# Kernel optimization log

Measured on AMD Instinct MI355X. Metric: run time of the kernel, lower is better.

## Reference

```python
import jax, jax.numpy as jnp
import numpy as np

N, D, H, E = 50000, 128, 128, 800000

def _layernorm(h, g, b, eps=1e-5):
    m = jnp.mean(h, axis=-1, keepdims=True)
    v = jnp.mean((h - m) ** 2, axis=-1, keepdims=True)
    return (h - m) * jax.lax.rsqrt(v + eps) * g + b

def setup_inputs() -> dict:
    key = jax.random.key(0)
    ks = jax.random.split(key, 24)
    s = 0.02
    inp = {
        "x": jax.random.normal(ks[0], (N, D), dtype=jnp.float32),
        "edge_index": jax.random.randint(ks[1], (2, E), 0, N, dtype=jnp.int64),
        "degree": jax.random.uniform(ks[2], (N, 1), dtype=jnp.float32) * 32.0,
        "W_lin": jax.random.normal(ks[3], (D, H), jnp.float32) * s,
        "b_lin": jnp.zeros((H,), jnp.float32),
        "Wa1": jax.random.normal(ks[4], (H, H), jnp.float32) * s,
        "ba1": jnp.zeros((H,), jnp.float32),
        "Wa2": jax.random.normal(ks[5], (H, H), jnp.float32) * s,
        "ba2": jnp.zeros((H,), jnp.float32),
        "Wb1": jax.random.normal(ks[6], (H, H), jnp.float32) * s,
        "bb1": jnp.zeros((H,), jnp.float32),
        "Wb2": jax.random.normal(ks[7], (H, H), jnp.float32) * s,
        "bb2": jnp.zeros((H,), jnp.float32),
        "Wg1": jax.random.normal(ks[8], (H, H), jnp.float32) * s,
        "bg1": jnp.zeros((H,), jnp.float32),
        "Wg2": jax.random.normal(ks[9], (H, H), jnp.float32) * s,
        "bg2": jnp.zeros((H,), jnp.float32),
        "Wf1": jax.random.normal(ks[10], (H, H), jnp.float32) * s,
        "bf1": jnp.zeros((H,), jnp.float32),
        "Wf2": jax.random.normal(ks[11], (H, H), jnp.float32) * s,
        "bf2": jnp.zeros((H,), jnp.float32),
        "ln_g": jnp.ones((H,), jnp.float32),
        "ln_b": jnp.zeros((H,), jnp.float32),
    }
    return inp

def reference(x, edge_index, degree, W_lin, b_lin, Wa1, ba1, Wa2, ba2,
              Wb1, bb1, Wb2, bb2, Wg1, bg1, Wg2, bg2, Wf1, bf1, Wf2, bf2,
              ln_g, ln_b):
    # Dropout layers are identity (eval mode)
    h = x @ W_lin + b_lin                                  # [N,H]
    x_res = _layernorm(h, ln_g, ln_b)
    alpha = jax.nn.softplus(jax.nn.relu(h @ Wa1 + ba1) @ Wa2 + ba2)
    beta = jax.nn.softplus(jax.nn.relu(h @ Wb1 + bb1) @ Wb2 + bb2)
    gamma = jax.nn.gelu(h @ Wg1 + bg1, approximate=False) @ Wg2 + bg2
    src, dst = edge_index[0], edge_index[1]
    agg = jax.ops.segment_sum(h[src], dst, num_segments=h.shape[0])  # [N,H]
    y = (beta * agg + gamma) / (alpha + beta * degree)
    z = jax.nn.gelu(y @ Wf1 + bf1, approximate=False) @ Wf2 + bf2
    return z + x_res
```

## Files before the change

### kernel.cpp

```cpp
#include <hip/hip_runtime.h>
#include <hip/hip_bf16.h>
#include <math.h>

#define NODES 50000
#define NEDGE 800000
#define NBLK_SCAN ((NODES + 255) / 256)
#define NT_TILES 782
#define NR_BLK 1563

typedef __bf16 bf16_t;
typedef __bf16 bf16x8 __attribute__((ext_vector_type(8)));
typedef float floatx4 __attribute__((ext_vector_type(4)));

__device__ __forceinline__ float bfbits2f(unsigned int hi16) {
    union { unsigned int u; float f; } c; c.u = hi16; return c.f;
}
__device__ __forceinline__ unsigned short f2bfbits(float f) {
    bf16_t b = (bf16_t)f; unsigned short u;
    __builtin_memcpy(&u, &b, 2); return u;
}

__device__ __forceinline__ float act_rt(float v, int act) {
    if (act == 1) return fmaxf(v, 0.f);
    if (act == 2) {
        float w = 0.79788456f * (v + 0.044715f * v * v * v);
        float e = __expf(2.f * w);
        float th = 1.f - 2.f / (e + 1.f);
        return 0.5f * v * (1.f + th);
    }
    if (act == 3) return fmaxf(v, 0.f) + __logf(1.f + __expf(-fabsf(v)));
    return v;
}

__global__ __launch_bounds__(256) void prep_w_zero(
    const float* __restrict__ w0, const float* __restrict__ w1,
    const float* __restrict__ w2, const float* __restrict__ w3,
    const float* __restrict__ w4, const float* __restrict__ w5,
    const float* __restrict__ w6, const float* __restrict__ w7,
    const float* __restrict__ w8, bf16_t* __restrict__ wt,
    int* __restrict__ cnt)
{
    if (blockIdx.x >= 9) {
        int i = (blockIdx.x - 9) * 256 + threadIdx.x;
        if (i < NODES) cnt[i] = 0;
        return;
    }
    const float* Ws[9] = {w0, w1, w2, w3, w4, w5, w6, w7, w8};
    const float* W = Ws[blockIdx.x];
    bf16_t* o = wt + blockIdx.x * 16384;
    for (int idx = threadIdx.x; idx < 16384; idx += 256) {
        int k = idx >> 7, n = idx & 127;
        o[n * 128 + k] = (bf16_t)W[idx];
    }
}

__device__ __forceinline__ void load_w_regs(const bf16_t* __restrict__ W,
                                            uint4 (&wr)[8], int t)
{
    for (int i = 0; i < 8; ++i) {
        int c = t + i * 256;
        int row = c >> 4, g = c & 15;
        wr[i] = *(const uint4*)(W + row * 128 + g * 8);
    }
}
__device__ __forceinline__ void store_w_regs(const uint4 (&wr)[8],
                                             bf16_t* Bs, int t)
{
    for (int i = 0; i < 8; ++i) {
        int c = t + i * 256;
        int row = c >> 4, g = c & 15;
        *(uint4*)&Bs[row * 128 + ((g ^ (row & 15)) * 8)] = wr[i];
    }
}
__device__ __forceinline__ void afrag_gbf16(const bf16_t* __restrict__ A,
        bf16x8 (&af)[4], int r0, int lane, int wave, int M)
{
    int gr = r0 + wave * 16 + (lane & 15);
    gr = min(gr, M - 1);
    const bf16_t* p = A + (size_t)gr * 128 + (lane >> 4) * 8;
    for (int kc = 0; kc < 4; ++kc)
        af[kc] = *(const bf16x8*)(p + kc * 32);
}
__device__ __forceinline__ void kloop64(const bf16x8 (&af)[4], const bf16_t* Bs,
                                        floatx4 (&acc)[8], int l15, int quad)
{
    for (int ni = 0; ni < 8; ++ni)
        for (int r = 0; r < 4; ++r) acc[ni][r] = 0.f;
    for (int kc = 0; kc < 4; ++kc) {
        int kg = kc * 4 + quad;
        bf16x8 b[8];
        for (int ni = 0; ni < 8; ++ni) {
            int row = ni * 16 + l15;
            b[ni] = *(const bf16x8*)&Bs[row * 128 + ((kg ^ l15) * 8)];
        }
        for (int ni = 0; ni < 8; ++ni)
            acc[ni] = __builtin_amdgcn_mfma_f32_16x16x32_bf16(
                af[kc], b[ni], acc[ni], 0, 0, 0);
    }
}
__device__ __forceinline__ void write_Csw(bf16_t* Csw, floatx4 (&acc)[8],
        const float (&bias_r)[8], int lane, int wave, int act)
{
    const int l15 = lane & 15, quad = lane >> 4;
    for (int ni = 0; ni < 8; ++ni) {
        int col = ni * 16 + l15;
        for (int r = 0; r < 4; ++r) {
            int row = wave * 16 + quad * 4 + r;
            float v = act_rt(acc[ni][r] + bias_r[ni], act);
            Csw[row * 128 + (((col >> 3) ^ (row & 15)) << 3) + (col & 7)] = (bf16_t)v;
        }
    }
}
__device__ __forceinline__ void afrag_Csw(const bf16_t* Csw, bf16x8 (&af)[4],
                                          int lane, int wave)
{
    int l15 = lane & 15, quad = lane >> 4;
    int row = wave * 16 + l15;
    for (int kc = 0; kc < 4; ++kc) {
        int kg = kc * 4 + quad;
        af[kc] = *(const bf16x8*)&Csw[row * 128 + ((kg ^ l15) * 8)];
    }
}
__device__ __forceinline__ void copy_Csw_out(const bf16_t* Csw,
        bf16_t* __restrict__ out, int t, int r0, int M)
{
    for (int i = 0; i < 4; ++i) {
        int c = t + i * 256;
        int row = c >> 4, g = c & 15;
        int gr = r0 + row;
        if (gr < M)
            *(uint4*)(out + (size_t)gr * 128 + g * 8) =
                *(const uint4*)&Csw[row * 128 + ((g ^ (row & 15)) * 8)];
    }
}

__global__ __launch_bounds__(256, 3) void hln_hist(
    const float* __restrict__ x, const bf16_t* __restrict__ wt,
    const float* __restrict__ b_lin,
    const float* __restrict__ ln_g, const float* __restrict__ ln_b,
    bf16_t* __restrict__ h, bf16_t* __restrict__ xres,
    const int* __restrict__ ei, int* __restrict__ cnt, int M)
{
    __shared__ __align__(16) char smem[49152];
    const int t = threadIdx.x;
    const int g = blockIdx.x >> 1;

    if (blockIdx.x & 1) {
        int base = g * 1024;
        for (int i = 0; i < 4; ++i) {
            int e = base + i * 256 + t;
            if (e < NEDGE) atomicAdd(&cnt[ei[NEDGE + e]], 1);
        }
        return;
    }

    bf16_t* Bs  = (bf16_t*)smem;
    bf16_t* Csw = (bf16_t*)(smem + 32768);
    const int r0 = g * 64;
    const int lane = t & 63, wave = t >> 6, l15 = lane & 15, quad = lane >> 4;
    uint4 wr[8];
    bf16x8 af[4];
    floatx4 acc[8];
    float bias_r[8];
    for (int ni = 0; ni < 8; ++ni) bias_r[ni] = b_lin[ni * 16 + l15];

    {
        int gr = min(r0 + wave * 16 + l15, M - 1);
        const float* p = x + (size_t)gr * 128 + quad * 8;
        for (int kc = 0; kc < 4; ++kc) {
            float4 u0 = *(const float4*)(p + kc * 32);
            float4 u1 = *(const float4*)(p + kc * 32 + 4);
            bf16x8 f;
            f[0] = (bf16_t)u0.x; f[1] = (bf16_t)u0.y;
            f[2] = (bf16_t)u0.z; f[3] = (bf16_t)u0.w;
            f[4] = (bf16_t)u1.x; f[5] = (bf16_t)u1.y;
            f[6] = (bf16_t)u1.z; f[7] = (bf16_t)u1.w;
            af[kc] = f;
        }
    }
    load_w_regs(wt, wr, t);
    store_w_regs(wr, Bs, t);
    __syncthreads();
    kloop64(af, Bs, acc, l15, quad);
    write_Csw(Csw, acc, bias_r, lane, wave, 0);
    __syncthreads();

    int row = t >> 2, p4 = t & 3;
    int gr = r0 + row;
    uint4 raw[4];
    float vals[32];
    float s = 0.f, sq = 0.f;
    for (int i = 0; i < 4; ++i) {
        int lg = p4 * 4 + i;
        raw[i] = *(const uint4*)&Csw[row * 128 + ((lg ^ (row & 15)) * 8)];
        const unsigned* u = (const unsigned*)&raw[i];
        for (int k = 0; k < 4; ++k) {
            float f0 = bfbits2f(u[k] << 16);
            float f1 = bfbits2f(u[k] & 0xffff0000u);
            vals[i * 8 + k * 2] = f0; vals[i * 8 + k * 2 + 1] = f1;
            s += f0 + f1; sq += f0 * f0 + f1 * f1;
        }
    }
    s += __shfl_xor(s, 1, 64);  sq += __shfl_xor(sq, 1, 64);
    s += __shfl_xor(s, 2, 64);  sq += __shfl_xor(sq, 2, 64);
    float m   = s * (1.f / 128.f);
    float var = fmaxf(sq * (1.f / 128.f) - m * m, 0.f);
    float rs  = rsqrtf(var + 1e-5f);
    if (gr < M) {
        for (int i = 0; i < 4; ++i) {
            int lg = p4 * 4 + i;
            *(uint4*)(h + (size_t)gr * 128 + lg * 8) = raw[i];
            unsigned short ob[8];
            for (int k = 0; k < 8; ++k) {
                int col = lg * 8 + k;
                ob[k] = f2bfbits((vals[i * 8 + k] - m) * rs * ln_g[col] + ln_b[col]);
            }
            uint4 o;
            o.x = ob[0] | ((unsigned)ob[1] << 16);
            o.y = ob[2] | ((unsigned)ob[3] << 16);
            o.z = ob[4] | ((unsigned)ob[5] << 16);
            o.w = ob[6] | ((unsigned)ob[7] << 16);
            *(uint4*)(xres + (size_t)gr * 128 + lg * 8) = o;
        }
    }
}

__global__ __launch_bounds__(256, 3) void branch_reorder(
    const bf16_t* __restrict__ h, const bf16_t* __restrict__ wt,
    const float* __restrict__ ba1, const float* __restrict__ ba2,
    const float* __restrict__ bb1, const float* __restrict__ bb2,
    const float* __restrict__ bg1, const float* __restrict__ bg2,
    bf16_t* __restrict__ al, bf16_t* __restrict__ be, bf16_t* __restrict__ ga,
    const int* __restrict__ ei, int* __restrict__ cur, int* __restrict__ srcs,
    int M)
{
    __shared__ __align__(16) char smem[49152];
    const int t = threadIdx.x;
    const int g5 = blockIdx.x / 5, r5 = blockIdx.x % 5;

    if (r5 >= 3) {
        int rb = g5 * 2 + (r5 - 3);
        int base = rb * 512;
        for (int i = 0; i < 2; ++i) {
            int e = base + i * 256 + t;
            if (e < NEDGE) {
                int dst = ei[NEDGE + e];
                int pos = atomicAdd(&cur[dst], 1);
                srcs[pos] = ei[e];
            }
        }
        return;
    }

    bf16_t* Bs  = (bf16_t*)smem;
    bf16_t* Csw = (bf16_t*)(smem + 32768);
    const int bb = g5 * 3 + r5;
    const int branch = bb / NT_TILES;
    const int r0 = (bb % NT_TILES) * 64;
    const int lane = t & 63, wave = t >> 6, l15 = lane & 15, quad = lane >> 4;
    uint4 wr[8];
    bf16x8 af[4];
    floatx4 acc[8];

    const bf16_t* w1 = wt + (1 + 2 * branch) * 16384;
    const bf16_t* w2 = wt + (2 + 2 * branch) * 16384;
    const float* b1p = (branch == 0) ? ba1 : (branch == 1) ? bb1 : bg1;
    const float* b2p = (branch == 0) ? ba2 : (branch == 1) ? bb2 : bg2;
    bf16_t* out = (branch == 0) ? al : (branch == 1) ? be : ga;
    const int act1 = (branch == 2) ? 2 : 1;
    const int act2 = (branch == 2) ? 0 : 3;

    float b1_r[8], b2_r[8];
    for (int ni = 0; ni < 8; ++ni) {
        b1_r[ni] = b1p[ni * 16 + l15];
        b2_r[ni] = b2p[ni * 16 + l15];
    }

    afrag_gbf16(h, af, r0, lane, wave, M);
    load_w_regs(w1, wr, t);
    store_w_regs(wr, Bs, t);
    load_w_regs(w2, wr, t);
    __syncthreads();

    kloop64(af, Bs, acc, l15, quad);
    write_Csw(Csw, acc, b1_r, lane, wave, act1);
    __syncthreads();
    store_w_regs(wr, Bs, t);
    __syncthreads();

    afrag_Csw(Csw, af, lane, wave);
    kloop64(af, Bs, acc, l15, quad);
    __syncthreads();
    write_Csw(Csw, acc, b2_r, lane, wave, act2);
    __syncthreads();
    copy_Csw_out(Csw, out, t, r0, M);
}

__global__ __launch_bounds__(256, 3) void fused_out(
    const bf16_t* __restrict__ y, const bf16_t* __restrict__ wt,
    const float* __restrict__ bf1, const float* __restrict__ bf2,
    const bf16_t* __restrict__ xres, float* __restrict__ out, int M)
{
    __shared__ __align__(16) char smem[49152];
    bf16_t* Bs  = (bf16_t*)smem;
    bf16_t* Csw = (bf16_t*)(smem + 32768);
    float*  Cf  = (float*)smem;
    const int t = threadIdx.x;
    const int r0 = blockIdx.x * 64;
    const int lane = t & 63, wave = t >> 6, l15 = lane & 15, quad = lane >> 4;
    uint4 wr[8];
    bf16x8 af[4];
    floatx4 acc[8];

    float b1_r[8], b2_r[8];
    for (int ni = 0; ni < 8; ++ni) {
        b1_r[ni] = bf1[ni * 16 + l15];
        b2_r[ni] = bf2[ni * 16 + l15];
    }

    afrag_gbf16(y, af, r0, lane, wave, M);
    load_w_regs(wt + 7 * 16384, wr, t);
    store_w_regs(wr, Bs, t);
    load_w_regs(wt + 8 * 16384, wr, t);
    __syncthreads();

    kloop64(af, Bs, acc, l15, quad);
    write_Csw(Csw, acc, b1_r, lane, wave, 2);
    __syncthreads();
    store_w_regs(wr, Bs, t);
    __syncthreads();

    afrag_Csw(Csw, af, lane, wave);
    kloop64(af, Bs, acc, l15, quad);
    __syncthreads();

    for (int ni = 0; ni < 8; ++ni) {
        int col = ni * 16 + l15;
        for (int r = 0; r < 4; ++r) {
            int row = wave * 16 + quad * 4 + r;
            Cf[row * 132 + col] = acc[ni][r] + b2_r[ni];
        }
    }
    __syncthreads();
    for (int i = 0; i < 8; ++i) {
        int c = t + i * 256;
        int row = c >> 5, q = c & 31;
        int gr = r0 + row;
        if (gr < M) {
            float4 v = *(const float4*)&Cf[row * 132 + q * 4];
            uint2 xr = *(const uint2*)(xres + (size_t)gr * 128 + q * 4);
            v.x += bfbits2f(xr.x << 16);
            v.y += bfbits2f(xr.x & 0xffff0000u);
            v.z += bfbits2f(xr.y << 16);
            v.w += bfbits2f(xr.y & 0xffff0000u);
            *(float4*)(out + (size_t)gr * 128 + q * 4) = v;
        }
    }
}

__global__ __launch_bounds__(256) void scan1_kernel(const int* __restrict__ cnt,
        int* __restrict__ offs, int* __restrict__ bsum)
{
    __shared__ int sd[256];
    int tid = threadIdx.x;
    int i = blockIdx.x * 256 + tid;
    int v = (i < NODES) ? cnt[i] : 0;
    sd[tid] = v;
    __syncthreads();
    for (int o = 1; o < 256; o <<= 1) {
        int other = (tid >= o) ? sd[tid - o] : 0;
        __syncthreads();
        sd[tid] += other;
        __syncthreads();
    }
    if (i < NODES) offs[i] = sd[tid] - v;
    if (tid == 255) bsum[blockIdx.x] = sd[255];
}

__global__ __launch_bounds__(256) void scan2_kernel(const int* __restrict__ bsum,
                                                    int* __restrict__ bofs)
{
    __shared__ int sd[256];
    int tid = threadIdx.x;
    int v = (tid < NBLK_SCAN) ? bsum[tid] : 0;
    sd[tid] = v;
    __syncthreads();
    for (int o = 1; o < 256; o <<= 1) {
        int other = (tid >= o) ? sd[tid - o] : 0;
        __syncthreads();
        sd[tid] += other;
        __syncthreads();
    }
    if (tid < NBLK_SCAN) bofs[tid] = sd[tid] - v;
}

__global__ __launch_bounds__(256) void scan3_kernel(const int* __restrict__ offs,
        const int* __restrict__ bofs, int* __restrict__ off_start,
        int* __restrict__ cur)
{
    int i = blockIdx.x * 256 + threadIdx.x;
    if (i < NODES) {
        int v = offs[i] + bofs[blockIdx.x];
        off_start[i] = v;
        cur[i] = v;
    }
}

__global__ __launch_bounds__(256) void gather_y_kernel(
    const int* __restrict__ off_start, const int* __restrict__ cnt,
    const int* __restrict__ srcs, const bf16_t* __restrict__ h,
    const bf16_t* __restrict__ al, const bf16_t* __restrict__ be,
    const bf16_t* __restrict__ ga, const float* __restrict__ deg,
    bf16_t* __restrict__ y, int M)
{
    int wave = threadIdx.x >> 6, lane = threadIdx.x & 63;
    int node = blockIdx.x * 4 + wave;
    if (node >= M) return;
    int s0 = __builtin_amdgcn_readfirstlane(off_start[node]);
    int n  = __builtin_amdgcn_readfirstlane(cnt[node]);
    int grp = lane >> 4, c16 = lane & 15;
    float a[8] = {0.f, 0.f, 0.f, 0.f, 0.f, 0.f, 0.f, 0.f};

    for (int j = 0; j < n; j += 8) {
        int e0 = j + grp, e1 = j + 4 + grp;
        int i0 = srcs[s0 + min(e0, n - 1)];
        int i1 = srcs[s0 + min(e1, n - 1)];
        uint4 v0 = *(const uint4*)(h + (size_t)i0 * 128 + c16 * 8);
        uint4 v1 = *(const uint4*)(h + (size_t)i1 * 128 + c16 * 8);
        if (e0 < n) {
            const unsigned* u = (const unsigned*)&v0;
            for (int k = 0; k < 4; ++k) {
                a[2 * k]     += bfbits2f(u[k] << 16);
                a[2 * k + 1] += bfbits2f(u[k] & 0xffff0000u);
            }
        }
        if (e1 < n) {
            const unsigned* u = (const unsigned*)&v1;
            for (int k = 0; k < 4; ++k) {
                a[2 * k]     += bfbits2f(u[k] << 16);
                a[2 * k + 1] += bfbits2f(u[k] & 0xffff0000u);
            }
        }
    }
    for (int k = 0; k < 8; ++k) {
        a[k] += __shfl_xor(a[k], 16, 64);
        a[k] += __shfl_xor(a[k], 32, 64);
    }
    if (lane < 16) {
        size_t i0 = (size_t)node * 128 + (size_t)c16 * 8;
        uint4 ra = *(const uint4*)(al + i0);
        uint4 rb = *(const uint4*)(be + i0);
        uint4 rg = *(const uint4*)(ga + i0);
        float d = deg[node];
        const unsigned* ua = (const unsigned*)&ra;
        const unsigned* ub = (const unsigned*)&rb;
        const unsigned* ug = (const unsigned*)&rg;
        unsigned short o[8];
        for (int k = 0; k < 4; ++k) {
            float a0 = bfbits2f(ua[k] << 16), a1 = bfbits2f(ua[k] & 0xffff0000u);
            float b0 = bfbits2f(ub[k] << 16), b1 = bfbits2f(ub[k] & 0xffff0000u);
            float g0 = bfbits2f(ug[k] << 16), g1 = bfbits2f(ug[k] & 0xffff0000u);
            o[2 * k]     = f2bfbits((b0 * a[2 * k]     + g0) / (a0 + b0 * d));
            o[2 * k + 1] = f2bfbits((b1 * a[2 * k + 1] + g1) / (a1 + b1 * d));
        }
        uint4 ov;
        ov.x = o[0] | ((unsigned)o[1] << 16);
        ov.y = o[2] | ((unsigned)o[3] << 16);
        ov.z = o[4] | ((unsigned)o[5] << 16);
        ov.w = o[6] | ((unsigned)o[7] << 16);
        *(uint4*)(y + i0) = ov;
    }
}

extern "C" void kernel_launch(void* const* d_in, const int* in_sizes, int n_in,
                              void* d_out, int out_size, void* d_ws, size_t ws_size,
                              hipStream_t stream)
{
    const float* x    = (const float*)d_in[0];
    const int*   ei   = (const int*)d_in[1];
    const float* deg  = (const float*)d_in[2];
    const float* W_lin = (const float*)d_in[3];  const float* b_lin = (const float*)d_in[4];
    const float* Wa1 = (const float*)d_in[5];    const float* ba1 = (const float*)d_in[6];
    const float* Wa2 = (const float*)d_in[7];    const float* ba2 = (const float*)d_in[8];
    const float* Wb1 = (const float*)d_in[9];    const float* bb1 = (const float*)d_in[10];
    const float* Wb2 = (const float*)d_in[11];   const float* bb2 = (const float*)d_in[12];
    const float* Wg1 = (const float*)d_in[13];   const float* bg1 = (const float*)d_in[14];
    const float* Wg2 = (const float*)d_in[15];   const float* bg2 = (const float*)d_in[16];
    const float* Wf1 = (const float*)d_in[17];   const float* bf1 = (const float*)d_in[18];
    const float* Wf2 = (const float*)d_in[19];   const float* bf2 = (const float*)d_in[20];
    const float* ln_g = (const float*)d_in[21];  const float* ln_b = (const float*)d_in[22];

    const int M = NODES;
    const size_t NB2 = (size_t)M * 128 * 2;

    char* ws = (char*)d_ws;
    size_t off = 0;
    bf16_t* wt  = (bf16_t*)(ws + off); off += (size_t)9 * 16384 * 2;
    bf16_t* h   = (bf16_t*)(ws + off); off += NB2;
    bf16_t* al  = (bf16_t*)(ws + off); off += NB2;
    bf16_t* be  = (bf16_t*)(ws + off); off += NB2;
    bf16_t* ga  = (bf16_t*)(ws + off); off += NB2;
    bf16_t* yv  = (bf16_t*)(ws + off); off += NB2;
    bf16_t* xres = (bf16_t*)(ws + off); off += NB2;
    int* cnt       = (int*)(ws + off); off += (size_t)NODES * 4 + 64;
    int* offs      = (int*)(ws + off); off += (size_t)NODES * 4 + 64;
    int* off_start = (int*)(ws + off); off += (size_t)NODES * 4 + 64;
    int* cur       = (int*)(ws + off); off += (size_t)NODES * 4 + 64;
    int* bsum      = (int*)(ws + off); off += 256 * 4;
    int* bofs      = (int*)(ws + off); off += 256 * 4;
    int* srcs      = (int*)(ws + off); off += (size_t)NEDGE * 4;
    float* outp = (float*)d_out;

    dim3 blk(256);

    prep_w_zero<<<9 + NBLK_SCAN, blk, 0, stream>>>(
        W_lin, Wa1, Wa2, Wb1, Wb2, Wg1, Wg2, Wf1, Wf2, wt, cnt);

    hln_hist<<<2 * NT_TILES, blk, 0, stream>>>(
        x, wt, b_lin, ln_g, ln_b, h, xres, ei, cnt, M);

    scan1_kernel<<<NBLK_SCAN, blk, 0, stream>>>(cnt, offs, bsum);
    scan2_kernel<<<1, blk, 0, stream>>>(bsum, bofs);
    scan3_kernel<<<NBLK_SCAN, blk, 0, stream>>>(offs, bofs, off_start, cur);

    branch_reorder<<<5 * NT_TILES, blk, 0, stream>>>(
        h, wt, ba1, ba2, bb1, bb2, bg1, bg2, al, be, ga, ei, cur, srcs, M);

    gather_y_kernel<<<(M + 3) / 4, blk, 0, stream>>>(off_start, cnt, srcs, h,
                                                     al, be, ga, deg, yv, M);
    fused_out<<<NT_TILES, blk, 0, stream>>>(yv, wt, bf1, bf2, xres, outp, M);
}
```

Baseline: 305.5 us.

## Replace global CSR build with two-pass bucketed sort fused into GEMM kernels

The old CSR build used a per-node global atomic histogram, three scan kernels, and a global-atomic scatter. It is replaced by a two-pass bucket sort over 98 buckets of 512 destination nodes. Pass one runs inside the h/LayerNorm kernel: each block builds a shared-memory histogram, reserves space per bucket with one atomic, and writes packed (src, local dst) words to per-bucket buffers. Pass two runs inside the branch-MLP kernel: one block per bucket does a local counting sort in shared memory and emits node offsets, counts and sorted sources. This removes three launches and most contended global atomics. The cost is a fixed per-bucket capacity that silently drops edges if a bucket overflows, and source ids packed into 16 bits.

```diff
diff --git a/kernel.cpp b/kernel.cpp
--- a/kernel.cpp
+++ b/kernel.cpp
@@ -4,9 +4,12 @@
 
 #define NODES 50000
 #define NEDGE 800000
-#define NBLK_SCAN ((NODES + 255) / 256)
 #define NT_TILES 782
-#define NR_BLK 1563
+#define NBUCK 98
+#define BSHIFT 9
+#define BCAP 10240
+#define NP1 195
+#define EPB1 4104
 
 typedef __bf16 bf16_t;
 typedef __bf16 bf16x8 __attribute__((ext_vector_type(8)));
@@ -38,11 +41,10 @@
     const float* __restrict__ w4, const float* __restrict__ w5,
     const float* __restrict__ w6, const float* __restrict__ w7,
     const float* __restrict__ w8, bf16_t* __restrict__ wt,
-    int* __restrict__ cnt)
+    int* __restrict__ gcur)
 {
     if (blockIdx.x >= 9) {
-        int i = (blockIdx.x - 9) * 256 + threadIdx.x;
-        if (i < NODES) cnt[i] = 0;
+        if (threadIdx.x < NBUCK) gcur[threadIdx.x] = 0;
         return;
     }
     const float* Ws[9] = {w0, w1, w2, w3, w4, w5, w6, w7, w8};
@@ -134,29 +136,51 @@
     }
 }
 
-__global__ __launch_bounds__(256, 3) void hln_hist(
+__global__ __launch_bounds__(256, 3) void hln_p1(
     const float* __restrict__ x, const bf16_t* __restrict__ wt,
     const float* __restrict__ b_lin,
     const float* __restrict__ ln_g, const float* __restrict__ ln_b,
     bf16_t* __restrict__ h, bf16_t* __restrict__ xres,
-    const int* __restrict__ ei, int* __restrict__ cnt, int M)
+    const int* __restrict__ ei, int* __restrict__ gcur,
+    unsigned* __restrict__ ebuf, int M)
 {
     __shared__ __align__(16) char smem[49152];
     const int t = threadIdx.x;
-    const int g = blockIdx.x >> 1;
-
-    if (blockIdx.x & 1) {
-        int base = g * 1024;
-        for (int i = 0; i < 4; ++i) {
-            int e = base + i * 256 + t;
-            if (e < NEDGE) atomicAdd(&cnt[ei[NEDGE + e]], 1);
+    const int bid = blockIdx.x;
+
+    if (bid % 5 == 4) {
+        int* lcnt  = (int*)smem;
+        int* lbase = lcnt + NBUCK;
+        if (t < NBUCK) lcnt[t] = 0;
+        __syncthreads();
+        int p1id = bid / 5;
+        int base = p1id * EPB1;
+        int e_end = min(base + EPB1, NEDGE);
+        for (int e = base + t; e < e_end; e += 256)
+            atomicAdd(&lcnt[ei[NEDGE + e] >> BSHIFT], 1);
+        __syncthreads();
+        if (t < NBUCK) {
+            lbase[t] = atomicAdd(&gcur[t], lcnt[t]);
+            lcnt[t] = 0;
+        }
+        __syncthreads();
+        for (int e = base + t; e < e_end; e += 256) {
+            int d = ei[NEDGE + e];
+            int s = ei[e];
+            int b = d >> BSHIFT;
+            int off = atomicAdd(&lcnt[b], 1);
+            int pos = lbase[b] + off;
+            if (pos < BCAP)
+                ebuf[(size_t)b * BCAP + pos] =
+                    (unsigned)s | ((unsigned)(d & 511) << 16);
         }
         return;
     }
 
     bf16_t* Bs  = (bf16_t*)smem;
     bf16_t* Csw = (bf16_t*)(smem + 32768);
-    const int r0 = g * 64;
+    const int tile = bid - bid / 5;
+    const int r0 = tile * 64;
     const int lane = t & 63, wave = t >> 6, l15 = lane & 15, quad = lane >> 4;
     uint4 wr[8];
     bf16x8 af[4];
@@ -225,38 +249,75 @@
     }
 }
 
-__global__ __launch_bounds__(256, 3) void branch_reorder(
+__global__ __launch_bounds__(256, 3) void branch_p2(
     const bf16_t* __restrict__ h, const bf16_t* __restrict__ wt,
     const float* __restrict__ ba1, const float* __restrict__ ba2,
     const float* __restrict__ bb1, const float* __restrict__ bb2,
     const float* __restrict__ bg1, const float* __restrict__ bg2,
     bf16_t* __restrict__ al, bf16_t* __restrict__ be, bf16_t* __restrict__ ga,
-    const int* __restrict__ ei, int* __restrict__ cur, int* __restrict__ srcs,
-    int M)
+    const int* __restrict__ gcur, const unsigned* __restrict__ ebuf,
+    int* __restrict__ off_start, int* __restrict__ cntN,
+    int* __restrict__ srcs, int M)
 {
     __shared__ __align__(16) char smem[49152];
     const int t = threadIdx.x;
-    const int g5 = blockIdx.x / 5, r5 = blockIdx.x % 5;
-
-    if (r5 >= 3) {
-        int rb = g5 * 2 + (r5 - 3);
-        int base = rb * 512;
-        for (int i = 0; i < 2; ++i) {
-            int e = base + i * 256 + t;
-            if (e < NEDGE) {
-                int dst = ei[NEDGE + e];
-                int pos = atomicAdd(&cur[dst], 1);
-                srcs[pos] = ei[e];
+    const int bid = blockIdx.x;
+
+    if (bid % 25 == 24) {
+        int* ncnt = (int*)smem;
+        int* sa   = ncnt + 512;
+        int* sb   = sa + 512;
+        int* ncur = sb + 512;
+        int* red  = ncur + 512;
+        const int b = bid / 25;
+        int total = min(gcur[b], BCAP);
+
+        int v = 0;
+        for (int j = t; j < b; j += 256) v += min(gcur[j], BCAP);
+        for (int o = 1; o < 64; o <<= 1) v += __shfl_xor(v, o, 64);
+        if ((t & 63) == 0) red[t >> 6] = v;
+        ncnt[t] = 0; ncnt[t + 256] = 0;
+        __syncthreads();
+        int bucketBase = red[0] + red[1] + red[2] + red[3];
+
+        const unsigned* eb = ebuf + (size_t)b * BCAP;
+        for (int i = t; i < total; i += 256)
+            atomicAdd(&ncnt[eb[i] >> 16], 1);
+        __syncthreads();
+        sa[t] = ncnt[t]; sa[t + 256] = ncnt[t + 256];
+        __syncthreads();
+        int* pin = sa; int* pout = sb;
+        for (int o = 1; o < 512; o <<= 1) {
+            for (int j = t; j < 512; j += 256)
+                pout[j] = pin[j] + (j >= o ? pin[j - o] : 0);
+            __syncthreads();
+            int* tmp = pin; pin = pout; pout = tmp;
+        }
+        for (int j = t; j < 512; j += 256) {
+            int excl = pin[j] - ncnt[j];
+            int node = (b << BSHIFT) + j;
+            if (node < NODES) {
+                off_start[node] = bucketBase + excl;
+                cntN[node] = ncnt[j];
             }
+            ncur[j] = excl;
+        }
+        __syncthreads();
+        for (int i = t; i < total; i += 256) {
+            unsigned p = eb[i];
+            int dl = p >> 16;
+            int pos = atomicAdd(&ncur[dl], 1);
+            srcs[bucketBase + pos] = (int)(p & 0xFFFFu);
         }
         return;
     }
 
+    const int tile = bid - bid / 25;
+    if (tile >= 3 * NT_TILES) return;
     bf16_t* Bs  = (bf16_t*)smem;
     bf16_t* Csw = (bf16_t*)(smem + 32768);
-    const int bb = g5 * 3 + r5;
-    const int branch = bb / NT_TILES;
-    const int r0 = (bb % NT_TILES) * 64;
+    const int branch = tile / NT_TILES;
+    const int r0 = (tile % NT_TILES) * 64;
     const int lane = t & 63, wave = t >> 6, l15 = lane & 15, quad = lane >> 4;
     uint4 wr[8];
     bf16x8 af[4];
@@ -355,54 +416,6 @@
             v.w += bfbits2f(xr.y & 0xffff0000u);
             *(float4*)(out + (size_t)gr * 128 + q * 4) = v;
         }
-    }
-}
-
-__global__ __launch_bounds__(256) void scan1_kernel(const int* __restrict__ cnt,
-        int* __restrict__ offs, int* __restrict__ bsum)
-{
-    __shared__ int sd[256];
-    int tid = threadIdx.x;
-    int i = blockIdx.x * 256 + tid;
-    int v = (i < NODES) ? cnt[i] : 0;
-    sd[tid] = v;
-    __syncthreads();
-    for (int o = 1; o < 256; o <<= 1) {
-        int other = (tid >= o) ? sd[tid - o] : 0;
-        __syncthreads();
-        sd[tid] += other;
-        __syncthreads();
-    }
-    if (i < NODES) offs[i] = sd[tid] - v;
-    if (tid == 255) bsum[blockIdx.x] = sd[255];
-}
-
-__global__ __launch_bounds__(256) void scan2_kernel(const int* __restrict__ bsum,
-                                                    int* __restrict__ bofs)
-{
-    __shared__ int sd[256];
-    int tid = threadIdx.x;
-    int v = (tid < NBLK_SCAN) ? bsum[tid] : 0;
-    sd[tid] = v;
-    __syncthreads();
-    for (int o = 1; o < 256; o <<= 1) {
-        int other = (tid >= o) ? sd[tid - o] : 0;
-        __syncthreads();
-        sd[tid] += other;
-        __syncthreads();
-    }
-    if (tid < NBLK_SCAN) bofs[tid] = sd[tid] - v;
-}
-
-__global__ __launch_bounds__(256) void scan3_kernel(const int* __restrict__ offs,
-        const int* __restrict__ bofs, int* __restrict__ off_start,
-        int* __restrict__ cur)
-{
-    int i = blockIdx.x * 256 + threadIdx.x;
-    if (i < NODES) {
-        int v = offs[i] + bofs[blockIdx.x];
-        off_start[i] = v;
-        cur[i] = v;
     }
 }
 
@@ -502,31 +515,26 @@
     bf16_t* ga  = (bf16_t*)(ws + off); off += NB2;
     bf16_t* yv  = (bf16_t*)(ws + off); off += NB2;
     bf16_t* xres = (bf16_t*)(ws + off); off += NB2;
-    int* cnt       = (int*)(ws + off); off += (size_t)NODES * 4 + 64;
-    int* offs      = (int*)(ws + off); off += (size_t)NODES * 4 + 64;
+    int* gcur      = (int*)(ws + off); off += 128 * 4;
     int* off_start = (int*)(ws + off); off += (size_t)NODES * 4 + 64;
-    int* cur       = (int*)(ws + off); off += (size_t)NODES * 4 + 64;
-    int* bsum      = (int*)(ws + off); off += 256 * 4;
-    int* bofs      = (int*)(ws + off); off += 256 * 4;
+    int* cntN      = (int*)(ws + off); off += (size_t)NODES * 4 + 64;
     int* srcs      = (int*)(ws + off); off += (size_t)NEDGE * 4;
+    unsigned* ebuf = (unsigned*)(ws + off); off += (size_t)NBUCK * BCAP * 4;
     float* outp = (float*)d_out;
 
     dim3 blk(256);
 
-    prep_w_zero<<<9 + NBLK_SCAN, blk, 0, stream>>>(
-        W_lin, Wa1, Wa2, Wb1, Wb2, Wg1, Wg2, Wf1, Wf2, wt, cnt);
-
-    hln_hist<<<2 * NT_TILES, blk, 0, stream>>>(
-        x, wt, b_lin, ln_g, ln_b, h, xres, ei, cnt, M);
-
-    scan1_kernel<<<NBLK_SCAN, blk, 0, stream>>>(cnt, offs, bsum);
-    scan2_kernel<<<1, blk, 0, stream>>>(bsum, bofs);
-    scan3_kernel<<<NBLK_SCAN, blk, 0, stream>>>(offs, bofs, off_start, cur);
-
-    branch_reorder<<<5 * NT_TILES, blk, 0, stream>>>(
-        h, wt, ba1, ba2, bb1, bb2, bg1, bg2, al, be, ga, ei, cur, srcs, M);
-
-    gather_y_kernel<<<(M + 3) / 4, blk, 0, stream>>>(off_start, cnt, srcs, h,
+    prep_w_zero<<<10, blk, 0, stream>>>(
+        W_lin, Wa1, Wa2, Wb1, Wb2, Wg1, Wg2, Wf1, Wf2, wt, gcur);
+
+    hln_p1<<<977, blk, 0, stream>>>(
+        x, wt, b_lin, ln_g, ln_b, h, xres, ei, gcur, ebuf, M);
+
+    branch_p2<<<2450, blk, 0, stream>>>(
+        h, wt, ba1, ba2, bb1, bb2, bg1, bg2, al, be, ga,
+        gcur, ebuf, off_start, cntN, srcs, M);
+
+    gather_y_kernel<<<(M + 3) / 4, blk, 0, stream>>>(off_start, cntN, srcs, h,
                                                      al, be, ga, deg, yv, M);
     fused_out<<<NT_TILES, blk, 0, stream>>>(yv, wt, bf1, bf2, xres, outp, M);
 }
```

Result: faster. 282.2 us (-7.6%).
